# Optimization experiments

Measured on AMD Instinct MI355X. Metric: run time of the kernel, lower is better.

The kernel has to match this reference:

```python
import jax, jax.numpy as jnp
import numpy as np
from functools import partial

B, A = 256, 32          # batch_size, num_atoms
N = B * A               # total nodes = 8192
E = 262144              # edges
H = 128                 # hidden_dim
LD, AF = 64, 16         # latent_dim, atom_feature_dim
L = 6                   # num_layers
LN_EPS = 1e-5

silu = jax.nn.silu


def setup_inputs() -> dict:
    key = jax.random.key(0)
    ks = jax.random.split(key, 32)
    s = 0.02
    inp = {
        "z": jax.random.normal(ks[0], (B, LD), jnp.float32),
        "atom_types": jax.random.uniform(ks[1], (N, AF), jnp.float32),
        "pos_init": jax.random.normal(ks[2], (N, 3), jnp.float32) * 0.1,
        "edge_index": jax.random.randint(ks[3], (2, E), 0, N, jnp.int64) if jax.config.jax_enable_x64 else jax.random.randint(ks[3], (2, E), 0, N, jnp.int32),
        "batch": jax.random.randint(ks[4], (N,), 0, B, jnp.int32),
        # latent injector: (LD+AF)->2H -> 2H->H -> H->H
        "inj_W1": jax.random.normal(ks[5], (LD + AF, 2 * H), jnp.float32) * s,
        "inj_b1": jnp.zeros((2 * H,), jnp.float32),
        "inj_W2": jax.random.normal(ks[6], (2 * H, H), jnp.float32) * s,
        "inj_b2": jnp.zeros((H,), jnp.float32),
        "inj_W3": jax.random.normal(ks[7], (H, H), jnp.float32) * s,
        "inj_b3": jnp.zeros((H,), jnp.float32),
        # stacked per-layer params [L, ...]
        "edge_W1": jax.random.normal(ks[8], (L, 2 * H + 1, H), jnp.float32) * s,
        "edge_b1": jnp.zeros((L, H), jnp.float32),
        "edge_W2": jax.random.normal(ks[9], (L, H, H), jnp.float32) * s,
        "edge_b2": jnp.zeros((L, H), jnp.float32),
        "node_W1": jax.random.normal(ks[10], (L, 2 * H, H), jnp.float32) * s,
        "node_b1": jnp.zeros((L, H), jnp.float32),
        "node_W2": jax.random.normal(ks[11], (L, H, H), jnp.float32) * s,
        "node_b2": jnp.zeros((L, H), jnp.float32),
        "coord_W1": jax.random.normal(ks[12], (L, H, H), jnp.float32) * s,
        "coord_b1": jnp.zeros((L, H), jnp.float32),
        "coord_W2": jax.random.normal(ks[13], (L, H, 1), jnp.float32) * s,  # no bias
        "ln_g": jnp.ones((L, H), jnp.float32),
        "ln_b": jnp.zeros((L, H), jnp.float32),
    }
    return inp


def _layer_norm(x, g, b):
    mu = jnp.mean(x, axis=-1, keepdims=True)
    var = jnp.mean(jnp.square(x - mu), axis=-1, keepdims=True)
    return (x - mu) * jax.lax.rsqrt(var + LN_EPS) * g + b


def _egnn_forward(z, atom_types, pos_init, row, col,
                  inj_W1, inj_b1, inj_W2, inj_b2, inj_W3, inj_b3,
                  edge_W1, edge_b1, edge_W2, edge_b2,
                  node_W1, node_b1, node_W2, node_b2,
                  coord_W1, coord_b1, coord_W2, ln_g, ln_b):
    # latent injection
    z_exp = jnp.repeat(z, A, axis=0)                      # [N, LD]
    h0 = jnp.concatenate([atom_types, z_exp], axis=1)     # [N, AF+LD]
    h = silu(h0 @ inj_W1 + inj_b1)
    h = silu(h @ inj_W2 + inj_b2)
    h = h @ inj_W3 + inj_b3                               # [N, H]

    deg = jax.ops.segment_sum(jnp.ones((E,), h.dtype), row, num_segments=N)[:, None]  # [N,1]

    def step(carry, p):
        h, pos = carry
        (eW1, eb1, eW2, eb2, nW1, nb1, nW2, nb2, cW1, cb1, cW2, g, b) = p
        dpos = pos[row] - pos[col]                                   # [E,3]
        dist_sq = jnp.sum(jnp.square(dpos), axis=1, keepdims=True)   # [E,1]
        ef = jnp.concatenate([h[row], h[col], dist_sq], axis=1)      # [E,2H+1]
        m = silu(silu(ef @ eW1 + eb1) @ eW2 + eb2)                   # [E,H]
        cw = silu(m @ cW1 + cb1) @ cW2                               # [E,1]
        coord_update = jax.ops.segment_sum(cw * dpos, row, num_segments=N)  # [N,3]
        pos_new = pos + coord_update / (deg + 1e-6)
        agg = jax.ops.segment_sum(m, row, num_segments=N)            # [N,H]
        nu = silu(jnp.concatenate([h, agg], axis=1) @ nW1 + nb1) @ nW2 + nb2
        h_new = _layer_norm(h + nu, g, b)
        return (h_new, pos_new), None

    params = (edge_W1, edge_b1, edge_W2, edge_b2, node_W1, node_b1,
              node_W2, node_b2, coord_W1, coord_b1, coord_W2, ln_g, ln_b)
    (h, pos), _ = jax.lax.scan(step, (h, pos_init), params)
    return pos


def reference(z, atom_types, pos_init, edge_index, batch,
              inj_W1, inj_b1, inj_W2, inj_b2, inj_W3, inj_b3,
              edge_W1, edge_b1, edge_W2, edge_b2,
              node_W1, node_b1, node_W2, node_b2,
              coord_W1, coord_b1, coord_W2, ln_g, ln_b):
    row, col = edge_index[0], edge_index[1]
    return _egnn_forward(z, atom_types, pos_init, row, col,
                         inj_W1, inj_b1, inj_W2, inj_b2, inj_W3, inj_b3,
                         edge_W1, edge_b1, edge_W2, edge_b2,
                         node_W1, node_b1, node_W2, node_b2,
                         coord_W1, coord_b1, coord_W2, ln_g, ln_b)
```

## Files before the change

### kernel.cpp

```cpp
#include <hip/hip_runtime.h>
#include <hip/hip_bf16.h>

#define NNODES 8192
#define NEDGES 262144
#define HDIM 128
#define NLAYERS 6
#define NMASK (NNODES - 1)

typedef __attribute__((ext_vector_type(8))) short bf16x8;
typedef __attribute__((ext_vector_type(4))) float f32x4;
typedef const __attribute__((address_space(1))) void gvoid;
typedef __attribute__((address_space(3))) void svoid;

__device__ __forceinline__ float silu_f(float x) {
    return x * __builtin_amdgcn_rcpf(1.0f + __expf(-x));
}
__device__ __forceinline__ unsigned short f2bu(float x) {
    unsigned int u; __builtin_memcpy(&u, &x, 4);
    return (unsigned short)((u + 0x8000u) >> 16);
}
__device__ __forceinline__ float bu2f(unsigned short u) {
    unsigned int v = ((unsigned int)u) << 16;
    float f; __builtin_memcpy(&f, &v, 4);
    return f;
}

__device__ __forceinline__ void stage_slice(const unsigned short* src,
                                            unsigned short* dst, int w) {
    const unsigned short* s = src + w * 1024;
    unsigned short* d = dst + w * 1024;
    __builtin_amdgcn_global_load_lds((gvoid*)s, (svoid*)d, 16, 0, 0);
    __builtin_amdgcn_global_load_lds((gvoid*)(s + 512), (svoid*)(d + 512), 16, 0, 0);
}

__global__ void detect_kernel(const int* __restrict__ ei32, int* __restrict__ flags) {
    if (blockIdx.x == 0 && threadIdx.x == 0) {
        flags[1] = (ei32[1] == 0 && ei32[3] == 0 && ei32[5] == 0 && ei32[7] == 0) ? 1 : 0;
    }
}
__device__ __forceinline__ int load_idx(const void* ei, int is64, int i) {
    int v = is64 ? (int)(((const long long*)ei)[i]) : ((const int*)ei)[i];
    return v & NMASK;
}

__global__ void pos_init_kernel(const float* __restrict__ pin, float* __restrict__ pos) {
    int i = blockIdx.x * blockDim.x + threadIdx.x;
    if (i < NNODES * 3) pos[i] = pin[i];
}

__global__ void cnt_kernel(const void* __restrict__ ei, const int* __restrict__ flags,
                           int* __restrict__ cnt) {
    int i = blockIdx.x * blockDim.x + threadIdx.x;
    if (i < NEDGES) atomicAdd(&cnt[load_idx(ei, flags[1], i)], 1);
}
__global__ void scan_kernel(const int* __restrict__ cnt, int* __restrict__ woff,
                            float* __restrict__ deg) {
    __shared__ int sums[256];
    const int t = threadIdx.x;
    const int base = t * 32;
    int s = 0;
#pragma unroll
    for (int i = 0; i < 32; ++i) s += cnt[base + i];
    sums[t] = s;
    __syncthreads();
    if (t == 0) {
        int run = 0;
        for (int k = 0; k < 256; ++k) { int v = sums[k]; sums[k] = run; run += v; }
    }
    __syncthreads();
    int run = sums[t];
#pragma unroll
    for (int i = 0; i < 32; ++i) {
        int c = cnt[base + i];
        woff[base + i] = run;
        deg[base + i] = (float)c;
        run += c;
    }
}
__global__ void scatter_kernel(const void* __restrict__ ei, const int* __restrict__ flags,
                               int* __restrict__ woff,
                               int* __restrict__ rowS, int* __restrict__ colS) {
    int i = blockIdx.x * blockDim.x + threadIdx.x;
    if (i < NEDGES) {
        const int is64 = flags[1];
        int r = load_idx(ei, is64, i);
        int c = load_idx(ei, is64, NEDGES + i);
        int p = atomicAdd(&woff[r], 1);
        rowS[p] = r;
        colS[p] = c;
    }
}

__global__ void prep_weights_kernel(const float* __restrict__ eW1,
                                    const float* __restrict__ eW2,
                                    const float* __restrict__ cW1,
                                    const float* __restrict__ nW1,
                                    const float* __restrict__ nW2,
                                    unsigned short* __restrict__ ewt,
                                    unsigned short* __restrict__ n1tb,
                                    unsigned short* __restrict__ n2tb,
                                    float* __restrict__ w1d) {
    const int TB = NLAYERS * 8 * 4 * 128 * 8;
    const int TS = NLAYERS * 4 * 4 * 128 * 8;
    const int TD = NLAYERS * 128;
    const int TOT = 2 * TB + 3 * TS + TD;
    for (int i = blockIdx.x * blockDim.x + threadIdx.x; i < TOT;
         i += gridDim.x * blockDim.x) {
        if (i < TB) {
            int j = i & 7, r = i >> 3;
            int n = r & 127; r >>= 7;
            int ch = r & 3; r >>= 2;
            int sl = r & 7; int l = r >> 3;
            int k = sl * 32 + ch * 8 + j;
            ewt[(size_t)(l * 16 + sl) * 4096 + ch * 1024 + n * 8 + j] =
                f2bu(eW1[((size_t)l * 257 + k) * 128 + n]);
        } else if (i < TB + TS) {
            int q = i - TB;
            int j = q & 7, r = q >> 3;
            int n = r & 127; r >>= 7;
            int ch = r & 3; r >>= 2;
            int sl = r & 3; int l = r >> 2;
            int k = sl * 32 + ch * 8 + j;
            ewt[(size_t)(l * 16 + 8 + sl) * 4096 + ch * 1024 + n * 8 + j] =
                f2bu(eW2[((size_t)l * 128 + k) * 128 + n]);
        } else if (i < TB + 2 * TS) {
            int q = i - TB - TS;
            int j = q & 7, r = q >> 3;
            int n = r & 127; r >>= 7;
            int ch = r & 3; r >>= 2;
            int sl = r & 3; int l = r >> 2;
            int k = sl * 32 + ch * 8 + j;
            ewt[(size_t)(l * 16 + 12 + sl) * 4096 + ch * 1024 + n * 8 + j] =
                f2bu(cW1[((size_t)l * 128 + k) * 128 + n]);
        } else if (i < 2 * TB + 2 * TS) {
            int q = i - TB - 2 * TS;
            int j = q & 7, r = q >> 3;
            int n = r & 127; r >>= 7;
            int ch = r & 3; r >>= 2;
            int sl = r & 7; int l = r >> 3;
            int k = sl * 32 + ch * 8 + j;
            n1tb[q] = f2bu(nW1[((size_t)l * 256 + k) * 128 + n]);
        } else if (i < 2 * TB + 3 * TS) {
            int q = i - 2 * TB - 2 * TS;
            int j = q & 7, r = q >> 3;
            int n = r & 127; r >>= 7;
            int ch = r & 3; r >>= 2;
            int sl = r & 3; int l = r >> 2;
            int k = sl * 32 + ch * 8 + j;
            n2tb[q] = f2bu(nW2[((size_t)l * 128 + k) * 128 + n]);
        } else {
            int r = i - 2 * TB - 3 * TS, l = r / 128, n = r % 128;
            w1d[r] = eW1[((size_t)l * 257 + 256) * 128 + n];
        }
    }
}

__global__ __launch_bounds__(256) void inj_kernel(
    const float* __restrict__ atom, const float* __restrict__ z,
    const float* __restrict__ W1, const float* __restrict__ b1,
    const float* __restrict__ W2, const float* __restrict__ b2,
    const float* __restrict__ W3, const float* __restrict__ b3,
    unsigned short* __restrict__ hb)
{
    __shared__ __align__(16) float in_s[16][84];
    __shared__ __align__(16) float s1[16][260];
    __shared__ __align__(16) float s2[16][132];
    const int tid = threadIdx.x;
    const int n0 = blockIdx.x * 16;

    if (tid < 80) {
        for (int e = 0; e < 16; ++e) {
            int n = n0 + e;
            in_s[e][tid] = (tid < 16) ? atom[n * 16 + tid] : z[(n >> 5) * 64 + (tid - 16)];
        }
    }
    __syncthreads();
    {
        float acc[16];
        float bias = b1[tid];
#pragma unroll
        for (int e = 0; e < 16; ++e) acc[e] = bias;
        for (int k4 = 0; k4 < 20; ++k4) {
            float w0 = W1[(k4 * 4 + 0) * 256 + tid];
            float w1 = W1[(k4 * 4 + 1) * 256 + tid];
            float w2 = W1[(k4 * 4 + 2) * 256 + tid];
            float w3 = W1[(k4 * 4 + 3) * 256 + tid];
#pragma unroll
            for (int e = 0; e < 16; ++e) {
                const float4 v = *(const float4*)&in_s[e][k4 * 4];
                acc[e] += v.x * w0 + v.y * w1 + v.z * w2 + v.w * w3;
            }
        }
#pragma unroll
        for (int e = 0; e < 16; ++e) s1[e][tid] = silu_f(acc[e]);
    }
    __syncthreads();
    const int j = tid & 127, hv = tid >> 7;
    {
        float acc[8];
        float bias = b2[j];
#pragma unroll
        for (int e = 0; e < 8; ++e) acc[e] = bias;
        for (int k4 = 0; k4 < 64; ++k4) {
            float w0 = W2[(k4 * 4 + 0) * 128 + j];
            float w1 = W2[(k4 * 4 + 1) * 128 + j];
            float w2 = W2[(k4 * 4 + 2) * 128 + j];
            float w3 = W2[(k4 * 4 + 3) * 128 + j];
#pragma unroll
            for (int e = 0; e < 8; ++e) {
                const float4 v = *(const float4*)&s1[hv * 8 + e][k4 * 4];
                acc[e] += v.x * w0 + v.y * w1 + v.z * w2 + v.w * w3;
            }
        }
#pragma unroll
        for (int e = 0; e < 8; ++e) s2[hv * 8 + e][j] = silu_f(acc[e]);
    }
    __syncthreads();
    {
        float acc[8];
        float bias = b3[j];
#pragma unroll
        for (int e = 0; e < 8; ++e) acc[e] = bias;
        for (int k4 = 0; k4 < 32; ++k4) {
            float w0 = W3[(k4 * 4 + 0) * 128 + j];
            float w1 = W3[(k4 * 4 + 1) * 128 + j];
            float w2 = W3[(k4 * 4 + 2) * 128 + j];
            float w3 = W3[(k4 * 4 + 3) * 128 + j];
#pragma unroll
            for (int e = 0; e < 8; ++e) {
                const float4 v = *(const float4*)&s2[hv * 8 + e][k4 * 4];
                acc[e] += v.x * w0 + v.y * w1 + v.z * w2 + v.w * w3;
            }
        }
#pragma unroll
        for (int e = 0; e < 8; ++e)
            hb[(size_t)(n0 + hv * 8 + e) * HDIM + j] = f2bu(acc[e]);
    }
}

__global__ __launch_bounds__(64) void proj_kernel(
    const unsigned short* __restrict__ hb,
    const unsigned short* __restrict__ wt,
    const float* __restrict__ eb1,
    float* __restrict__ pt)
{
    const int tid = threadIdx.x;
    const int quad = tid >> 4, l16 = tid & 15;
    const int n0 = blockIdx.x * 16;

    const unsigned short* bbase = wt + quad * 1024 + l16 * 8;
    f32x4 acc[16];
    const f32x4 zero = {0.f, 0.f, 0.f, 0.f};
#pragma unroll
    for (int i = 0; i < 16; ++i) acc[i] = zero;

#pragma unroll
    for (int kc = 0; kc < 4; ++kc) {
        bf16x8 a = *(const bf16x8*)(hb + (size_t)(n0 + l16) * HDIM + kc * 32 + quad * 8);
#pragma unroll
        for (int nt = 0; nt < 8; ++nt) {
            bf16x8 bA = *(const bf16x8*)(bbase + kc * 4096 + nt * 128);
            bf16x8 bB = *(const bf16x8*)(bbase + (4 + kc) * 4096 + nt * 128);
            acc[nt]     = __builtin_amdgcn_mfma_f32_16x16x32_bf16(a, bA, acc[nt], 0, 0, 0);
            acc[8 + nt] = __builtin_amdgcn_mfma_f32_16x16x32_bf16(a, bB, acc[8 + nt], 0, 0, 0);
        }
    }
#pragma unroll
    for (int nt = 0; nt < 8; ++nt) {
        const int j = nt * 16 + l16;
        const float bias = eb1[j];
#pragma unroll
        for (int r = 0; r < 4; ++r) {
            const int m = quad * 4 + r;
            pt[(size_t)(n0 + m) * 256 + j]       = acc[nt][r] + bias;
            pt[(size_t)(n0 + m) * 256 + 128 + j] = acc[8 + nt][r];
        }
    }
}

__global__ __launch_bounds__(256, 3) void edge_mfma_kernel(
    const float* __restrict__ pt, const float* __restrict__ pos,
    const int* __restrict__ rowS, const int* __restrict__ colS,
    const unsigned short* __restrict__ wt,
    const float* __restrict__ w1d,
    const float* __restrict__ eb2,
    const float* __restrict__ cb1, const float* __restrict__ cw2,
    float* __restrict__ agg, float* __restrict__ cu)
{
    __shared__ __align__(16) unsigned short Cbuf[128][136];
    __shared__ __align__(16) unsigned short Bbuf[2][4096];

    const int tid = threadIdx.x;
    const int e0 = blockIdx.x * 128;
    const int L = tid & 63;
    const int w = tid >> 6;
    const int quad = L >> 4, l16 = L & 15;
    const int m0 = w * 32;

    stage_slice(wt, Bbuf[0], w);

    if (tid < 128) {
        int r = rowS[e0 + tid], c = colS[e0 + tid];
        float dx = pos[r * 3 + 0] - pos[c * 3 + 0];
        float dy = pos[r * 3 + 1] - pos[c * 3 + 1];
        float dz = pos[r * 3 + 2] - pos[c * 3 + 2];
        *(float*)&Cbuf[tid][128] = dx * dx + dy * dy + dz * dz;
        Cbuf[tid][130] = (unsigned short)r;
        Cbuf[tid][131] = (unsigned short)c;
        Cbuf[tid][132] = f2bu(dx); Cbuf[tid][133] = f2bu(dy); Cbuf[tid][134] = f2bu(dz);
    }
    __syncthreads();

    stage_slice(wt + 4096, Bbuf[1], w);

    {
        const int e = tid >> 1;
        const int ch0 = (tid & 1) * 64;
        const int rr = Cbuf[e][130];
        const int cc = Cbuf[e][131];
        const float dsq = *(const float*)&Cbuf[e][128];
        const float* p1p = pt + (size_t)rr * 256 + ch0;
        const float* p2p = pt + (size_t)cc * 256 + 128 + ch0;
#pragma unroll
        for (int v = 0; v < 16; ++v) {
            const float4 pa = *(const float4*)(p1p + v * 4);
            const float4 pb = *(const float4*)(p2p + v * 4);
            const float4 wv = *(const float4*)(w1d + ch0 + v * 4);
            short4 o;
            o.x = (short)f2bu(silu_f(pa.x + pb.x + dsq * wv.x));
            o.y = (short)f2bu(silu_f(pa.y + pb.y + dsq * wv.y));
            o.z = (short)f2bu(silu_f(pa.z + pb.z + dsq * wv.z));
            o.w = (short)f2bu(silu_f(pa.w + pb.w + dsq * wv.w));
            *(short4*)&Cbuf[e][ch0 + v * 4] = o;
        }
    }

    f32x4 acc[2][8];
    const f32x4 zero = {0.f, 0.f, 0.f, 0.f};
#pragma unroll
    for (int mt = 0; mt < 2; ++mt)
#pragma unroll
        for (int nt = 0; nt < 8; ++nt) acc[mt][nt] = zero;

#pragma unroll
    for (int s = 0; s < 8; ++s) {
        if (s) {
            __syncthreads();
            if (s < 7) stage_slice(wt + (s + 1) * 4096, Bbuf[(s + 1) & 1], w);
        }
        const unsigned short* bp = Bbuf[s & 1] + quad * 1024;
        const int kk = (s & 3) * 32 + quad * 8;
        bf16x8 a0 = *(const bf16x8*)&Cbuf[m0 + l16][kk];
        bf16x8 a1 = *(const bf16x8*)&Cbuf[m0 + 16 + l16][kk];
#pragma unroll
        for (int nt = 0; nt < 8; ++nt) {
            bf16x8 b = *(const bf16x8*)&bp[(nt * 16 + l16) * 8];
            acc[0][nt] = __builtin_amdgcn_mfma_f32_16x16x32_bf16(a0, b, acc[0][nt], 0, 0, 0);
            acc[1][nt] = __builtin_amdgcn_mfma_f32_16x16x32_bf16(a1, b, acc[1][nt], 0, 0, 0);
        }

        if (s == 3) {
#pragma unroll
            for (int nt = 0; nt < 8; ++nt) {
                const int n = nt * 16 + l16;
                const float bias = eb2[n];
#pragma unroll
                for (int mt = 0; mt < 2; ++mt)
#pragma unroll
                    for (int r = 0; r < 4; ++r) {
                        const int m = m0 + mt * 16 + quad * 4 + r;
                        Cbuf[m][n] = f2bu(silu_f(acc[mt][nt][r] + bias));
                    }
            }
#pragma unroll
            for (int mt = 0; mt < 2; ++mt)
#pragma unroll
                for (int nt = 0; nt < 8; ++nt) acc[mt][nt] = zero;
        }
    }

    {
        float s[2][4] = {{0.f, 0.f, 0.f, 0.f}, {0.f, 0.f, 0.f, 0.f}};
#pragma unroll
        for (int nt = 0; nt < 8; ++nt) {
            const int n = nt * 16 + l16;
            const float bias = cb1[n];
            const float wv = cw2[n];
#pragma unroll
            for (int mt = 0; mt < 2; ++mt)
#pragma unroll
                for (int r = 0; r < 4; ++r)
                    s[mt][r] += silu_f(acc[mt][nt][r] + bias) * wv;
        }
#pragma unroll
        for (int mt = 0; mt < 2; ++mt)
#pragma unroll
            for (int r = 0; r < 4; ++r) {
                float v = s[mt][r];
                v += __shfl_xor(v, 1);
                v += __shfl_xor(v, 2);
                v += __shfl_xor(v, 4);
                v += __shfl_xor(v, 8);
                if (l16 == 0)
                    *(float*)&Cbuf[m0 + mt * 16 + quad * 4 + r][128] = v;
            }
    }

    if (L < 32) {
        const int e = m0 + L;
        const int row = Cbuf[e][130];
        const float cwv = *(const float*)&Cbuf[e][128];
        float vx = cwv * bu2f(Cbuf[e][132]);
        float vy = cwv * bu2f(Cbuf[e][133]);
        float vz = cwv * bu2f(Cbuf[e][134]);
#pragma unroll
        for (int d = 1; d < 32; d <<= 1) {
            float ux = __shfl_up(vx, d);
            float uy = __shfl_up(vy, d);
            float uz = __shfl_up(vz, d);
            int rup = __shfl_up(row, d);
            if (L >= d && rup == row) { vx += ux; vy += uy; vz += uz; }
        }
        int rdn = __shfl_down(row, 1);
        if (L == 31 || rdn != row) {
            atomicAdd(&cu[row * 3 + 0], vx);
            atomicAdd(&cu[row * 3 + 1], vy);
            atomicAdd(&cu[row * 3 + 2], vz);
        }
    }

    {
        const int p = L;
        const int eb = m0;
        const int i31 = L & 31;
        const int myrow = Cbuf[eb + i31][130];
        const int prow = __shfl_up(myrow, 1);
        unsigned long long bm64 = __ballot(i31 != 0 && myrow != prow);
        unsigned int bm = (unsigned int)bm64;
        int curr = Cbuf[eb][130];
        float s0 = 0.0f, s1 = 0.0f;
#pragma unroll
        for (int i = 0; i < 32; ++i) {
            unsigned int v = *(const unsigned int*)&Cbuf[eb + i][2 * p];
            if (i && (bm & (1u << i))) {
                atomicAdd(&agg[(size_t)curr * HDIM + 2 * p], s0);
                atomicAdd(&agg[(size_t)curr * HDIM + 2 * p + 1], s1);
                s0 = 0.0f; s1 = 0.0f;
                curr = __shfl(myrow, i);
            }
            s0 += bu2f((unsigned short)(v & 0xffffu));
            s1 += bu2f((unsigned short)(v >> 16));
        }
        atomicAdd(&agg[(size_t)curr * HDIM + 2 * p], s0);
        atomicAdd(&agg[(size_t)curr * HDIM + 2 * p + 1], s1);
    }
}

__global__ __launch_bounds__(128) void node_mfma_kernel(
    const unsigned short* __restrict__ hb,
    float* __restrict__ agg,
    float* __restrict__ cu, const float* __restrict__ deg,
    const unsigned short* __restrict__ n1tb,
    const unsigned short* __restrict__ n2tb,
    const float* __restrict__ b1, const float* __restrict__ b2,
    const float* __restrict__ lg, const float* __restrict__ lb,
    unsigned short* __restrict__ h2b,
    float* __restrict__ pos)
{
    __shared__ __align__(16) unsigned short Cbuf[16][136];
    __shared__ float sLN[2][16][2];
    const int tid = threadIdx.x;
    const int n0 = blockIdx.x * 16;

    if (tid < 16) {
        int n = n0 + tid;
        float inv = __builtin_amdgcn_rcpf(deg[n] + 1e-6f);
        pos[n * 3 + 0] += cu[n * 3 + 0] * inv;
        pos[n * 3 + 1] += cu[n * 3 + 1] * inv;
        pos[n * 3 + 2] += cu[n * 3 + 2] * inv;
        cu[n * 3 + 0] = 0.0f;
        cu[n * 3 + 1] = 0.0f;
        cu[n * 3 + 2] = 0.0f;
    }

    const int L = tid & 63, w = tid >> 6;
    const int quad = L >> 4, l16 = L & 15;
    const int row = n0 + l16;
    const int nb = w * 64;

    f32x4 acc[4];
    const f32x4 zero = {0.f, 0.f, 0.f, 0.f};

#pragma unroll
    for (int nt = 0; nt < 4; ++nt) acc[nt] = zero;
#pragma unroll
    for (int kc = 0; kc < 8; ++kc) {
        bf16x8 a;
        if (kc < 4) {
            const int kk = kc * 32 + quad * 8;
            a = *(const bf16x8*)(hb + (size_t)row * HDIM + kk);
        } else {
            const int kk = (kc - 4) * 32 + quad * 8;
            const float4* p = (const float4*)(agg + (size_t)row * HDIM + kk);
            float4 u0 = p[0], u1 = p[1];
            a[0] = (short)f2bu(u0.x); a[1] = (short)f2bu(u0.y);
            a[2] = (short)f2bu(u0.z); a[3] = (short)f2bu(u0.w);
            a[4] = (short)f2bu(u1.x); a[5] = (short)f2bu(u1.y);
            a[6] = (short)f2bu(u1.z); a[7] = (short)f2bu(u1.w);
        }
        const unsigned short* bp = n1tb + (kc * 4 + quad) * 1024 + (nb + l16) * 8;
#pragma unroll
        for (int nt = 0; nt < 4; ++nt) {
            bf16x8 b = *(const bf16x8*)(bp + nt * 128);
            acc[nt] = __builtin_amdgcn_mfma_f32_16x16x32_bf16(a, b, acc[nt], 0, 0, 0);
        }
    }
    {
        const float4 z4 = {0.f, 0.f, 0.f, 0.f};
        float4* ap = (float4*)(agg + (size_t)(n0 + (tid >> 3)) * HDIM + (tid & 7) * 16);
#pragma unroll
        for (int i = 0; i < 4; ++i) ap[i] = z4;
    }
#pragma unroll
    for (int nt = 0; nt < 4; ++nt) {
        const int n = nb + nt * 16 + l16;
        const float bias = b1[n];
#pragma unroll
        for (int r = 0; r < 4; ++r)
            Cbuf[quad * 4 + r][n] = f2bu(silu_f(acc[nt][r] + bias));
    }
    __syncthreads();

#pragma unroll
    for (int nt = 0; nt < 4; ++nt) acc[nt] = zero;
#pragma unroll
    for (int kc = 0; kc < 4; ++kc) {
        const int kk = kc * 32 + quad * 8;
        bf16x8 a = *(const bf16x8*)&Cbuf[l16][kk];
        const unsigned short* bp = n2tb + (kc * 4 + quad) * 1024 + (nb + l16) * 8;
#pragma unroll
        for (int nt = 0; nt < 4; ++nt) {
            bf16x8 b = *(const bf16x8*)(bp + nt * 128);
            acc[nt] = __builtin_amdgcn_mfma_f32_16x16x32_bf16(a, b, acc[nt], 0, 0, 0);
        }
    }

#pragma unroll
    for (int nt = 0; nt < 4; ++nt) {
        const int n = nb + nt * 16 + l16;
        const float bias = b2[n];
#pragma unroll
        for (int r = 0; r < 4; ++r) {
            const int m = quad * 4 + r;
            acc[nt][r] += bias + bu2f(hb[(size_t)(n0 + m) * HDIM + n]);
        }
    }
#pragma unroll
    for (int r = 0; r < 4; ++r) {
        float s = 0.0f, ss = 0.0f;
#pragma unroll
        for (int nt = 0; nt < 4; ++nt) {
            float x = acc[nt][r];
            s += x; ss += x * x;
        }
#pragma unroll
        for (int d = 1; d < 16; d <<= 1) {
            s += __shfl_xor(s, d);
            ss += __shfl_xor(ss, d);
        }
        if (l16 == 0) {
            sLN[w][quad * 4 + r][0] = s;
            sLN[w][quad * 4 + r][1] = ss;
        }
    }
    __syncthreads();
#pragma unroll
    for (int r = 0; r < 4; ++r) {
        const int m = quad * 4 + r;
        float s = sLN[0][m][0] + sLN[1][m][0];
        float ss = sLN[0][m][1] + sLN[1][m][1];
        float mu = s * (1.0f / 128.0f);
        float var = ss * (1.0f / 128.0f) - mu * mu;
        float rs = rsqrtf(fmaxf(var, 0.0f) + 1e-5f);
#pragma unroll
        for (int nt = 0; nt < 4; ++nt) {
            const int n = nb + nt * 16 + l16;
            float val = (acc[nt][r] - mu) * rs * lg[n] + lb[n];
            h2b[(size_t)(n0 + m) * HDIM + n] = f2bu(val);
        }
    }
}

extern "C" void kernel_launch(void* const* d_in, const int* in_sizes, int n_in,
                              void* d_out, int out_size, void* d_ws, size_t ws_size,
                              hipStream_t stream) {
    const float* zF    = (const float*)d_in[0];
    const float* atomF = (const float*)d_in[1];
    const float* posI  = (const float*)d_in[2];
    const void*  ei    = d_in[3];
    const float* iW1 = (const float*)d_in[5];  const float* ib1 = (const float*)d_in[6];
    const float* iW2 = (const float*)d_in[7];  const float* ib2 = (const float*)d_in[8];
    const float* iW3 = (const float*)d_in[9];  const float* ib3 = (const float*)d_in[10];
    const float* eW1 = (const float*)d_in[11]; const float* eb1 = (const float*)d_in[12];
    const float* eW2 = (const float*)d_in[13]; const float* eb2 = (const float*)d_in[14];
    const float* nW1 = (const float*)d_in[15]; const float* nb1 = (const float*)d_in[16];
    const float* nW2 = (const float*)d_in[17]; const float* nb2 = (const float*)d_in[18];
    const float* cW1 = (const float*)d_in[19]; const float* cb1 = (const float*)d_in[20];
    const float* cW2 = (const float*)d_in[21];
    const float* lng = (const float*)d_in[22]; const float* lnb = (const float*)d_in[23];

    float* pos = (float*)d_out;

    float* ws = (float*)d_ws;
    int* flags = (int*)d_ws;
    size_t cur = 16;
    auto carve = [&](size_t n) { float* p = ws + cur; cur += n; return p; };
    float* deg  = carve(NNODES);
    float* cu   = carve((size_t)NNODES * 3);
    float* agg  = carve((size_t)NNODES * HDIM);
    unsigned short* hbA = (unsigned short*)carve((size_t)NNODES * HDIM / 2);
    unsigned short* hbB = (unsigned short*)carve((size_t)NNODES * HDIM / 2);
    float* pt   = carve((size_t)NNODES * 256);
    unsigned short* ewt  = (unsigned short*)carve((size_t)NLAYERS * 16 * 4096 / 2);
    unsigned short* n1tb = (unsigned short*)carve((size_t)NLAYERS * 8 * 4096 / 2);
    unsigned short* n2tb = (unsigned short*)carve((size_t)NLAYERS * 4 * 4096 / 2);
    float* w1d  = carve(NLAYERS * 128);
    int* cnt    = (int*)carve(NNODES);
    int* woff   = (int*)carve(NNODES);
    int* rowS   = (int*)carve(NEDGES);
    int* colS   = (int*)carve(NEDGES);

    detect_kernel<<<1, 64, 0, stream>>>((const int*)ei, flags);
    pos_init_kernel<<<(NNODES * 3 + 255) / 256, 256, 0, stream>>>(posI, pos);

    hipMemsetAsync(cnt, 0, NNODES * sizeof(int), stream);
    cnt_kernel<<<NEDGES / 256, 256, 0, stream>>>(ei, flags, cnt);
    scan_kernel<<<1, 256, 0, stream>>>(cnt, woff, deg);
    scatter_kernel<<<NEDGES / 256, 256, 0, stream>>>(ei, flags, woff, rowS, colS);

    prep_weights_kernel<<<2691, 256, 0, stream>>>(eW1, eW2, cW1, nW1, nW2,
                                                  ewt, n1tb, n2tb, w1d);
    inj_kernel<<<NNODES / 16, 256, 0, stream>>>(atomF, zF, iW1, ib1, iW2, ib2, iW3, ib3,
                                                hbA);

    hipMemsetAsync(agg, 0, (size_t)NNODES * HDIM * sizeof(float), stream);
    hipMemsetAsync(cu, 0, (size_t)NNODES * 3 * sizeof(float), stream);

    unsigned short* hb = hbA;
    unsigned short* ob = hbB;
    proj_kernel<<<NNODES / 16, 64, 0, stream>>>(hbA, ewt, eb1, pt);
    for (int l = 0; l < NLAYERS; ++l) {
        edge_mfma_kernel<<<NEDGES / 128, 256, 0, stream>>>(
            pt, pos, rowS, colS,
            ewt + (size_t)l * 16 * 4096 + 8 * 4096,
            w1d + (size_t)l * 128,
            eb2 + l * 128, cb1 + l * 128, cW2 + l * 128,
            agg, cu);
        node_mfma_kernel<<<NNODES / 16, 128, 0, stream>>>(
            hb, agg, cu, deg,
            n1tb + (size_t)l * 8 * 4096,
            n2tb + (size_t)l * 4 * 4096,
            nb1 + l * 128, nb2 + l * 128,
            lng + l * 128, lnb + l * 128,
            ob, pos);
        if (l < NLAYERS - 1)
            proj_kernel<<<NNODES / 16, 64, 0, stream>>>(
                ob, ewt + (size_t)(l + 1) * 16 * 4096, eb1 + (l + 1) * 128, pt);
        unsigned short* tb = hb; hb = ob; ob = tb;
    }
}
```

Measured before the change: 716.4 us.

## Fuse next-layer edge projection into node kernel and widen node/proj blocks

The per-layer proj_kernel launch is folded into node_mfma_kernel. The freshly layer-normed h is kept in shared memory and multiplied by the next layer's edge W1 halves to write pt directly, which removes one launch per layer and a global re-read of h. The node and proj kernels move from 64/128 to 256 threads, splitting output columns across four waves to raise parallelism per block. The edge kernel now loads its row/col indices straight from global memory before the first barrier, instead of reading them back from shared memory afterwards. The node kernel takes on extra register and shared-memory pressure and one more barrier in exchange.

```diff
diff --git a/kernel.cpp b/kernel.cpp
--- a/kernel.cpp
+++ b/kernel.cpp
@@ -238,43 +238,41 @@
     }
 }
 
-__global__ __launch_bounds__(64) void proj_kernel(
+__global__ __launch_bounds__(256) void proj_kernel(
     const unsigned short* __restrict__ hb,
     const unsigned short* __restrict__ wt,
     const float* __restrict__ eb1,
     float* __restrict__ pt)
 {
     const int tid = threadIdx.x;
-    const int quad = tid >> 4, l16 = tid & 15;
+    const int L = tid & 63, w = tid >> 6;
+    const int quad = L >> 4, l16 = L & 15;
     const int n0 = blockIdx.x * 16;
-
-    const unsigned short* bbase = wt + quad * 1024 + l16 * 8;
-    f32x4 acc[16];
+    const int colbase = (w & 1) * 64;
+    const int half = w >> 1;
+
+    f32x4 acc[4];
     const f32x4 zero = {0.f, 0.f, 0.f, 0.f};
 #pragma unroll
-    for (int i = 0; i < 16; ++i) acc[i] = zero;
+    for (int i = 0; i < 4; ++i) acc[i] = zero;
 
 #pragma unroll
     for (int kc = 0; kc < 4; ++kc) {
         bf16x8 a = *(const bf16x8*)(hb + (size_t)(n0 + l16) * HDIM + kc * 32 + quad * 8);
 #pragma unroll
-        for (int nt = 0; nt < 8; ++nt) {
-            bf16x8 bA = *(const bf16x8*)(bbase + kc * 4096 + nt * 128);
-            bf16x8 bB = *(const bf16x8*)(bbase + (4 + kc) * 4096 + nt * 128);
-            acc[nt]     = __builtin_amdgcn_mfma_f32_16x16x32_bf16(a, bA, acc[nt], 0, 0, 0);
-            acc[8 + nt] = __builtin_amdgcn_mfma_f32_16x16x32_bf16(a, bB, acc[8 + nt], 0, 0, 0);
-        }
-    }
-#pragma unroll
-    for (int nt = 0; nt < 8; ++nt) {
-        const int j = nt * 16 + l16;
-        const float bias = eb1[j];
-#pragma unroll
-        for (int r = 0; r < 4; ++r) {
-            const int m = quad * 4 + r;
-            pt[(size_t)(n0 + m) * 256 + j]       = acc[nt][r] + bias;
-            pt[(size_t)(n0 + m) * 256 + 128 + j] = acc[8 + nt][r];
-        }
+        for (int nt = 0; nt < 4; ++nt) {
+            const int j = colbase + nt * 16 + l16;
+            bf16x8 b = *(const bf16x8*)(wt + (size_t)(half * 4 + kc) * 4096 + quad * 1024 + j * 8);
+            acc[nt] = __builtin_amdgcn_mfma_f32_16x16x32_bf16(a, b, acc[nt], 0, 0, 0);
+        }
+    }
+#pragma unroll
+    for (int nt = 0; nt < 4; ++nt) {
+        const int j = colbase + nt * 16 + l16;
+        const float bias = half ? 0.0f : eb1[j];
+#pragma unroll
+        for (int r = 0; r < 4; ++r)
+            pt[(size_t)(n0 + quad * 4 + r) * 256 + half * 128 + j] = acc[nt][r] + bias;
     }
 }
 
@@ -297,6 +295,11 @@
     const int quad = L >> 4, l16 = L & 15;
     const int m0 = w * 32;
 
+    const int eA = tid >> 1;
+    const int ch0 = (tid & 1) * 64;
+    const int rrA = rowS[e0 + eA];
+    const int ccA = colS[e0 + eA];
+
     stage_slice(wt, Bbuf[0], w);
 
     if (tid < 128) {
@@ -314,13 +317,9 @@
     stage_slice(wt + 4096, Bbuf[1], w);
 
     {
-        const int e = tid >> 1;
-        const int ch0 = (tid & 1) * 64;
-        const int rr = Cbuf[e][130];
-        const int cc = Cbuf[e][131];
-        const float dsq = *(const float*)&Cbuf[e][128];
-        const float* p1p = pt + (size_t)rr * 256 + ch0;
-        const float* p2p = pt + (size_t)cc * 256 + 128 + ch0;
+        const float dsq = *(const float*)&Cbuf[eA][128];
+        const float* p1p = pt + (size_t)rrA * 256 + ch0;
+        const float* p2p = pt + (size_t)ccA * 256 + 128 + ch0;
 #pragma unroll
         for (int v = 0; v < 16; ++v) {
             const float4 pa = *(const float4*)(p1p + v * 4);
@@ -331,7 +330,7 @@
             o.y = (short)f2bu(silu_f(pa.y + pb.y + dsq * wv.y));
             o.z = (short)f2bu(silu_f(pa.z + pb.z + dsq * wv.z));
             o.w = (short)f2bu(silu_f(pa.w + pb.w + dsq * wv.w));
-            *(short4*)&Cbuf[e][ch0 + v * 4] = o;
+            *(short4*)&Cbuf[eA][ch0 + v * 4] = o;
         }
     }
 
@@ -456,7 +455,7 @@
     }
 }
 
-__global__ __launch_bounds__(128) void node_mfma_kernel(
+__global__ __launch_bounds__(256) void node_mfma_kernel(
     const unsigned short* __restrict__ hb,
     float* __restrict__ agg,
     float* __restrict__ cu, const float* __restrict__ deg,
@@ -465,10 +464,13 @@
     const float* __restrict__ b1, const float* __restrict__ b2,
     const float* __restrict__ lg, const float* __restrict__ lb,
     unsigned short* __restrict__ h2b,
-    float* __restrict__ pos)
+    float* __restrict__ pos,
+    const unsigned short* __restrict__ ewtN,
+    const float* __restrict__ eb1N,
+    float* __restrict__ pt, const int doProj)
 {
     __shared__ __align__(16) unsigned short Cbuf[16][136];
-    __shared__ float sLN[2][16][2];
+    __shared__ float sLN[4][16][2];
     const int tid = threadIdx.x;
     const int n0 = blockIdx.x * 16;
 
@@ -486,13 +488,13 @@
     const int L = tid & 63, w = tid >> 6;
     const int quad = L >> 4, l16 = L & 15;
     const int row = n0 + l16;
-    const int nb = w * 64;
-
-    f32x4 acc[4];
+    const int nb = w * 32;
+
+    f32x4 acc[2];
     const f32x4 zero = {0.f, 0.f, 0.f, 0.f};
 
 #pragma unroll
-    for (int nt = 0; nt < 4; ++nt) acc[nt] = zero;
+    for (int nt = 0; nt < 2; ++nt) acc[nt] = zero;
 #pragma unroll
     for (int kc = 0; kc < 8; ++kc) {
         bf16x8 a;
@@ -508,45 +510,45 @@
             a[4] = (short)f2bu(u1.x); a[5] = (short)f2bu(u1.y);
             a[6] = (short)f2bu(u1.z); a[7] = (short)f2bu(u1.w);
         }
-        const unsigned short* bp = n1tb + (kc * 4 + quad) * 1024 + (nb + l16) * 8;
-#pragma unroll
-        for (int nt = 0; nt < 4; ++nt) {
-            bf16x8 b = *(const bf16x8*)(bp + nt * 128);
+        const unsigned short* bp = n1tb + (kc * 4 + quad) * 1024;
+#pragma unroll
+        for (int nt = 0; nt < 2; ++nt) {
+            bf16x8 b = *(const bf16x8*)(bp + (nb + nt * 16 + l16) * 8);
             acc[nt] = __builtin_amdgcn_mfma_f32_16x16x32_bf16(a, b, acc[nt], 0, 0, 0);
         }
     }
+#pragma unroll
+    for (int nt = 0; nt < 2; ++nt) {
+        const int n = nb + nt * 16 + l16;
+        const float bias = b1[n];
+#pragma unroll
+        for (int r = 0; r < 4; ++r)
+            Cbuf[quad * 4 + r][n] = f2bu(silu_f(acc[nt][r] + bias));
+    }
+    __syncthreads();
+
     {
         const float4 z4 = {0.f, 0.f, 0.f, 0.f};
-        float4* ap = (float4*)(agg + (size_t)(n0 + (tid >> 3)) * HDIM + (tid & 7) * 16);
-#pragma unroll
-        for (int i = 0; i < 4; ++i) ap[i] = z4;
-    }
-#pragma unroll
-    for (int nt = 0; nt < 4; ++nt) {
-        const int n = nb + nt * 16 + l16;
-        const float bias = b1[n];
-#pragma unroll
-        for (int r = 0; r < 4; ++r)
-            Cbuf[quad * 4 + r][n] = f2bu(silu_f(acc[nt][r] + bias));
-    }
-    __syncthreads();
-
-#pragma unroll
-    for (int nt = 0; nt < 4; ++nt) acc[nt] = zero;
+        float4* ap = (float4*)(agg + (size_t)(n0 + (tid >> 4)) * HDIM + (tid & 15) * 8);
+        ap[0] = z4; ap[1] = z4;
+    }
+
+#pragma unroll
+    for (int nt = 0; nt < 2; ++nt) acc[nt] = zero;
 #pragma unroll
     for (int kc = 0; kc < 4; ++kc) {
         const int kk = kc * 32 + quad * 8;
         bf16x8 a = *(const bf16x8*)&Cbuf[l16][kk];
-        const unsigned short* bp = n2tb + (kc * 4 + quad) * 1024 + (nb + l16) * 8;
-#pragma unroll
-        for (int nt = 0; nt < 4; ++nt) {
-            bf16x8 b = *(const bf16x8*)(bp + nt * 128);
+        const unsigned short* bp = n2tb + (kc * 4 + quad) * 1024;
+#pragma unroll
+        for (int nt = 0; nt < 2; ++nt) {
+            bf16x8 b = *(const bf16x8*)(bp + (nb + nt * 16 + l16) * 8);
             acc[nt] = __builtin_amdgcn_mfma_f32_16x16x32_bf16(a, b, acc[nt], 0, 0, 0);
         }
     }
 
 #pragma unroll
-    for (int nt = 0; nt < 4; ++nt) {
+    for (int nt = 0; nt < 2; ++nt) {
         const int n = nb + nt * 16 + l16;
         const float bias = b2[n];
 #pragma unroll
@@ -559,7 +561,7 @@
     for (int r = 0; r < 4; ++r) {
         float s = 0.0f, ss = 0.0f;
 #pragma unroll
-        for (int nt = 0; nt < 4; ++nt) {
+        for (int nt = 0; nt < 2; ++nt) {
             float x = acc[nt][r];
             s += x; ss += x * x;
         }
@@ -574,19 +576,49 @@
         }
     }
     __syncthreads();
+
 #pragma unroll
     for (int r = 0; r < 4; ++r) {
         const int m = quad * 4 + r;
-        float s = sLN[0][m][0] + sLN[1][m][0];
-        float ss = sLN[0][m][1] + sLN[1][m][1];
+        float s = sLN[0][m][0] + sLN[1][m][0] + sLN[2][m][0] + sLN[3][m][0];
+        float ss = sLN[0][m][1] + sLN[1][m][1] + sLN[2][m][1] + sLN[3][m][1];
         float mu = s * (1.0f / 128.0f);
         float var = ss * (1.0f / 128.0f) - mu * mu;
         float rs = rsqrtf(fmaxf(var, 0.0f) + 1e-5f);
 #pragma unroll
-        for (int nt = 0; nt < 4; ++nt) {
+        for (int nt = 0; nt < 2; ++nt) {
             const int n = nb + nt * 16 + l16;
             float val = (acc[nt][r] - mu) * rs * lg[n] + lb[n];
-            h2b[(size_t)(n0 + m) * HDIM + n] = f2bu(val);
+            unsigned short vb = f2bu(val);
+            h2b[(size_t)(n0 + m) * HDIM + n] = vb;
+            Cbuf[m][n] = vb;
+        }
+    }
+
+    if (doProj) {
+        __syncthreads();
+        const int colbase = (w & 1) * 64;
+        const int half = w >> 1;
+        f32x4 pacc[4];
+#pragma unroll
+        for (int i = 0; i < 4; ++i) pacc[i] = zero;
+#pragma unroll
+        for (int kc = 0; kc < 4; ++kc) {
+            bf16x8 a = *(const bf16x8*)&Cbuf[l16][kc * 32 + quad * 8];
+#pragma unroll
+            for (int nt = 0; nt < 4; ++nt) {
+                const int j = colbase + nt * 16 + l16;
+                bf16x8 b = *(const bf16x8*)(ewtN + (size_t)(half * 4 + kc) * 4096 + quad * 1024 + j * 8);
+                pacc[nt] = __builtin_amdgcn_mfma_f32_16x16x32_bf16(a, b, pacc[nt], 0, 0, 0);
+            }
+        }
+#pragma unroll
+        for (int nt = 0; nt < 4; ++nt) {
+            const int j = colbase + nt * 16 + l16;
+            const float bias = half ? 0.0f : eb1N[j];
+#pragma unroll
+            for (int r = 0; r < 4; ++r)
+                pt[(size_t)(n0 + quad * 4 + r) * 256 + half * 128 + j] = pacc[nt][r] + bias;
         }
     }
 }
@@ -648,7 +680,7 @@
 
     unsigned short* hb = hbA;
     unsigned short* ob = hbB;
-    proj_kernel<<<NNODES / 16, 64, 0, stream>>>(hbA, ewt, eb1, pt);
+    proj_kernel<<<NNODES / 16, 256, 0, stream>>>(hbA, ewt, eb1, pt);
     for (int l = 0; l < NLAYERS; ++l) {
         edge_mfma_kernel<<<NEDGES / 128, 256, 0, stream>>>(
             pt, pos, rowS, colS,
@@ -656,16 +688,16 @@
             w1d + (size_t)l * 128,
             eb2 + l * 128, cb1 + l * 128, cW2 + l * 128,
             agg, cu);
-        node_mfma_kernel<<<NNODES / 16, 128, 0, stream>>>(
+        const int ln = (l < NLAYERS - 1) ? (l + 1) : l;
+        node_mfma_kernel<<<NNODES / 16, 256, 0, stream>>>(
             hb, agg, cu, deg,
             n1tb + (size_t)l * 8 * 4096,
             n2tb + (size_t)l * 4 * 4096,
             nb1 + l * 128, nb2 + l * 128,
             lng + l * 128, lnb + l * 128,
-            ob, pos);
-        if (l < NLAYERS - 1)
-            proj_kernel<<<NNODES / 16, 64, 0, stream>>>(
-                ob, ewt + (size_t)(l + 1) * 16 * 4096, eb1 + (l + 1) * 128, pt);
+            ob, pos,
+            ewt + (size_t)ln * 16 * 4096, eb1 + ln * 128, pt,
+            (l < NLAYERS - 1) ? 1 : 0);
         unsigned short* tb = hb; hb = ob; ob = tb;
     }
 }
```

New measurement: 656.2 us. -8.4%, faster.
